# Optimization experiments

Hardware: AMD Instinct MI355X
Metric: run time of the kernel (lower is better)

The kernel has to match this reference:

```python
import jax, jax.numpy as jnp
import numpy as np

KERNEL = 7
DS_LIM = 0.01
ALPHA_M = 1.0


def _smooth_field(field):
    # field [3,D,H,W] -> depthwise mean filter with kernel 7, SAME padding
    k = KERNEL
    w = jnp.ones((3, 1, k, k, k), dtype=field.dtype) / (k ** 3)
    out = jax.lax.conv_general_dilated(
        field[None], w, (1, 1, 1), 'SAME',
        dimension_numbers=('NCDHW', 'OIDHW', 'NCDHW'),
        feature_group_count=3)
    return out[0]


def _trilinear(vol, coords):
    # vol [B,D,H,W]; coords [B,3,D,H,W] in voxel units
    B, D, H, W = vol.shape
    cz = jnp.clip(coords[:, 0], 0.0, D - 1.0)
    cy = jnp.clip(coords[:, 1], 0.0, H - 1.0)
    cx = jnp.clip(coords[:, 2], 0.0, W - 1.0)
    z0 = jnp.floor(cz).astype(jnp.int32); z1 = jnp.minimum(z0 + 1, D - 1)
    y0 = jnp.floor(cy).astype(jnp.int32); y1 = jnp.minimum(y0 + 1, H - 1)
    x0 = jnp.floor(cx).astype(jnp.int32); x1 = jnp.minimum(x0 + 1, W - 1)
    fz = cz - z0; fy = cy - y0; fx = cx - x0
    b = jnp.arange(B)[:, None, None, None]
    g = lambda zi, yi, xi: vol[b, zi, yi, xi]
    c00 = g(z0, y0, x0) * (1 - fx) + g(z0, y0, x1) * fx
    c01 = g(z0, y1, x0) * (1 - fx) + g(z0, y1, x1) * fx
    c10 = g(z1, y0, x0) * (1 - fx) + g(z1, y0, x1) * fx
    c11 = g(z1, y1, x0) * (1 - fx) + g(z1, y1, x1) * fx
    c0 = c00 * (1 - fy) + c01 * fy
    c1 = c10 * (1 - fy) + c11 * fy
    return c0 * (1 - fz) + c1 * fz


def setup_inputs() -> dict:
    key = jax.random.key(0)
    ks = jax.random.split(key, 8)
    B, C, L = 8, 128, 5
    D = H = W = 96
    return {
        'encode_ds': jax.random.normal(ks[0], (B, C, L, L, L), jnp.float32),
        'orig': jax.random.normal(ks[1], (B, 1, D, H, W), jnp.float32),
        'mask': jax.random.uniform(ks[2], (B, 1, D, H, W), jnp.float32),
        'c1_w': jax.random.normal(ks[3], (1, C, 1, 1, 1), jnp.float32) * 0.05,
        'c1_b': jnp.zeros((1,), jnp.float32),
        'f1_w': jax.random.normal(ks[4], (1, L ** 3), jnp.float32) * 0.1,
        'f1_b': jnp.zeros((1,), jnp.float32),
        'offset_field': jax.random.normal(ks[5], (3, D, H, W), jnp.float32),
    }


def reference(encode_ds, orig, mask, c1_w, c1_b, f1_w, f1_b, offset_field):
    B = encode_ds.shape[0]
    # 1x1x1 Conv3d (128 -> 1) is a per-voxel channel contraction
    a = jnp.einsum('bcdhw,c->bdhw', encode_ds, c1_w[0, :, 0, 0, 0]) + c1_b[0]
    a = a.reshape(B, -1)                                   # [B, 125]
    alpha = jax.nn.sigmoid(a @ f1_w[0] + f1_b[0]) * ALPHA_M  # [B]

    # deform: smoothed, ds_lim-clamped offset field scaled by per-sample alpha
    field = jnp.clip(_smooth_field(offset_field), -DS_LIM, DS_LIM)  # [3,D,H,W]
    _, _, D, H, W = orig.shape
    base = jnp.stack(jnp.meshgrid(jnp.arange(D, dtype=orig.dtype),
                                  jnp.arange(H, dtype=orig.dtype),
                                  jnp.arange(W, dtype=orig.dtype),
                                  indexing='ij'))          # [3,D,H,W]
    scale = jnp.array([D, H, W], orig.dtype).reshape(1, 3, 1, 1, 1)
    disp = alpha[:, None, None, None, None] * field[None] * scale  # [B,3,D,H,W]
    coords = base[None] + disp

    def_ = _trilinear(orig[:, 0], coords)[:, None]
    mask_d = _trilinear(mask[:, 0], coords)[:, None]
    return def_, mask_d
```

## Files before the change

kernel.cpp:

```cpp
#include <hip/hip_runtime.h>
#include <hip/hip_fp16.h>
#include <math.h>

#define DD 96
#define VOX (96*96*96)
#define NB 8
#define NC 128
#define L3 125

#define BTS 16
#define BNT 6
#define BNTILE (BNT*BNT*BNT)
#define BHS 22
#define YBS 23

#define TZ 12
#define TY 8
#define TX 32
#define NTZ 8
#define NTY 12
#define NTX 3
#define STILE (NTZ*NTY*NTX)
#define HZS 14
#define HYS 10
#define HXS 34
#define HXP 35
#define HN (HZS*HYS*HXS)
#define HLDS (HZS*HYS*HXP)

typedef float vfloat2 __attribute__((ext_vector_type(2)));

static __device__ __forceinline__ vfloat2 h2f(__half2 h) {
    float2 t = __half22float2(h);
    vfloat2 r; r.x = t.x; r.y = t.y;
    return r;
}

__global__ __launch_bounds__(256) void blur_alpha(
        const float* __restrict__ in, float* __restrict__ out,
        const float* __restrict__ enc,
        const float* __restrict__ c1_w, const float* __restrict__ c1_b,
        const float* __restrict__ f1_w, const float* __restrict__ f1_b,
        float* __restrict__ alpha) {
    __shared__ float h[BHS * BHS * BHS];
    __shared__ float zb[BTS * BHS * BHS];
    __shared__ float red[4];
    float* yb = h;
    int tid = threadIdx.x;

    if (blockIdx.x >= 3 * BNTILE) {
        int b = blockIdx.x - 3 * BNTILE;
        const float4* e4 = (const float4*)(enc + (size_t)b * NC * L3);
        float s = 0.f;
        for (int j = tid; j < (NC * L3) / 4; j += 256) {
            float4 v = e4[j];
            int f = j * 4;
            s += v.x * c1_w[(f + 0) / L3] * f1_w[(f + 0) % L3];
            s += v.y * c1_w[(f + 1) / L3] * f1_w[(f + 1) % L3];
            s += v.z * c1_w[(f + 2) / L3] * f1_w[(f + 2) % L3];
            s += v.w * c1_w[(f + 3) / L3] * f1_w[(f + 3) % L3];
        }
        for (int off = 32; off > 0; off >>= 1) s += __shfl_down(s, off, 64);
        int lane = tid & 63, wid = tid >> 6;
        if (lane == 0) red[wid] = s;
        __syncthreads();
        if (tid == 0) {
            float tot = red[0] + red[1] + red[2] + red[3];
            float fwsum = 0.f;
            for (int v = 0; v < L3; ++v) fwsum += f1_w[v];
            float x = tot + c1_b[0] * fwsum + f1_b[0];
            alpha[b] = 1.f / (1.f + expf(-x));
        }
        return;
    }

    int blk = blockIdx.x;
    int c = blk / BNTILE;
    int t = blk % BNTILE;
    int tz = t / (BNT * BNT), ty = (t / BNT) % BNT, tx = t % BNT;
    int bz = tz * BTS, by = ty * BTS, bx = tx * BTS;
    const float* ib = in + (size_t)c * VOX;

    for (int i = tid; i < BHS * BHS * BHS; i += 256) {
        int hz = i / (BHS * BHS);
        int hy = (i / BHS) % BHS;
        int hx = i % BHS;
        int gz = bz + hz - 3, gy = by + hy - 3, gx = bx + hx - 3;
        float v = 0.f;
        if (gz >= 0 && gz < DD && gy >= 0 && gy < DD && gx >= 0 && gx < DD)
            v = ib[(gz * DD + gy) * DD + gx];
        h[i] = v;
    }
    __syncthreads();

    for (int cc = tid; cc < BHS * BHS; cc += 256) {
        float s = 0.f;
        #pragma unroll
        for (int z = 0; z < 7; ++z) s += h[z * (BHS * BHS) + cc];
        zb[cc] = s;
        for (int z = 1; z < BTS; ++z) {
            s += h[(z + 6) * (BHS * BHS) + cc] - h[(z - 1) * (BHS * BHS) + cc];
            zb[z * (BHS * BHS) + cc] = s;
        }
    }
    __syncthreads();

    for (int cc = tid; cc < BTS * BHS; cc += 256) {
        int z = cc / BHS, hx = cc % BHS;
        const float* zp = zb + z * (BHS * BHS) + hx;
        float s = 0.f;
        #pragma unroll
        for (int y = 0; y < 7; ++y) s += zp[y * BHS];
        yb[(z * BTS) * YBS + hx] = s;
        for (int y = 1; y < BTS; ++y) {
            s += zp[(y + 6) * BHS] - zp[(y - 1) * BHS];
            yb[(z * BTS + y) * YBS + hx] = s;
        }
    }
    __syncthreads();

    {
        int z = tid >> 4, y = tid & 15;
        const float* yp = yb + (z * BTS + y) * YBS;
        float* op = out + (size_t)c * VOX + ((bz + z) * DD + (by + y)) * DD + bx;
        float s = yp[0] + yp[1] + yp[2] + yp[3] + yp[4] + yp[5] + yp[6];
        #pragma unroll
        for (int xq = 0; xq < 4; ++xq) {
            float4 o4;
            #pragma unroll
            for (int j = 0; j < 4; ++j) {
                int x = xq * 4 + j;
                float v = s * (1.0f / 343.0f);
                v = fminf(fmaxf(v, -0.01f), 0.01f) * 96.0f;
                if (j == 0) o4.x = v; else if (j == 1) o4.y = v;
                else if (j == 2) o4.z = v; else o4.w = v;
                if (x < BTS - 1) s += yp[x + 7] - yp[x];
            }
            ((float4*)op)[xq] = o4;
        }
    }
}

__global__ __launch_bounds__(256, 8) void sample_tile(
        const float* __restrict__ orig,
        const float* __restrict__ mask,
        const float* __restrict__ field,
        const float* __restrict__ alpha,
        float* __restrict__ out) {
    __shared__ __half2 tile[HLDS];

    int blk = blockIdx.x;
    int b = blk / STILE;
    int r = blk % STILE;
    int o = r & 7;
    int l = r >> 3;
    int zh = o >> 2;
    int yq = o & 3;
    int lz4 = l / 9, ly3 = (l / 3) % 3, lx3 = l % 3;
    int tz = zh * 4 + lz4;
    int ty = yq * 3 + ly3;
    int tx = lx3;
    int bz = tz * TZ, by = ty * TY, bx = tx * TX;

    const float* ob = orig + (size_t)b * VOX;
    const float* mb = mask + (size_t)b * VOX;
    int tid = threadIdx.x;

    for (int i = tid; i < HN; i += 256) {
        int hz = i / (HYS * HXS);
        int rr = i - hz * (HYS * HXS);
        int hy = rr / HXS;
        int hx = rr - hy * HXS;
        int gz = min(max(bz + hz - 1, 0), DD - 1);
        int gy = min(max(by + hy - 1, 0), DD - 1);
        int gx = min(max(bx + hx - 1, 0), DD - 1);
        int g = (gz * DD + gy) * DD + gx;
        tile[(hz * HYS + hy) * HXP + hx] = __floats2half2_rn(ob[g], mb[g]);
    }
    float a = alpha[b];
    __syncthreads();

    const float2* fz2 = (const float2*)field;
    const float2* fy2 = (const float2*)(field + VOX);
    const float2* fx2 = (const float2*)(field + 2 * VOX);
    vfloat2* oD = (vfloat2*)(out);
    vfloat2* oM = (vfloat2*)(out + (size_t)NB * VOX);

    int lz  = tid >> 7;
    int ly  = (tid >> 4) & 7;
    int lxp = tid & 15;
    int gy  = by + ly;
    int gx0 = bx + 2 * lxp;
    float gyf = (float)gy;
    float gx0f = (float)gx0, gx1f = (float)(gx0 + 1);
    float c1z = (float)(1 - bz), c1y = (float)(1 - by), c1x = (float)(1 - bx);

    auto samp = [&](float gzf, float dzv, float dyv, float dxv,
                    float gxf) -> vfloat2 {
        float cz = fminf(fmaxf(fmaf(a, dzv, gzf), 0.f), (float)(DD - 1)) + c1z;
        float cy = fminf(fmaxf(fmaf(a, dyv, gyf), 0.f), (float)(DD - 1)) + c1y;
        float cx = fminf(fmaxf(fmaf(a, dxv, gxf), 0.f), (float)(DD - 1)) + c1x;
        float flz = floorf(cz), fly = floorf(cy), flx = floorf(cx);
        float fzf = cz - flz, fyf = cy - fly, fxf = cx - flx;
        int iz = (int)flz, iy = (int)fly, ix = (int)flx;

        const __half2* tp = tile + (iz * HYS + iy) * HXP + ix;
        vfloat2 v000 = h2f(tp[0]);
        vfloat2 v001 = h2f(tp[1]);
        vfloat2 v010 = h2f(tp[HXP]);
        vfloat2 v011 = h2f(tp[HXP + 1]);
        vfloat2 v100 = h2f(tp[HYS * HXP]);
        vfloat2 v101 = h2f(tp[HYS * HXP + 1]);
        vfloat2 v110 = h2f(tp[(HYS + 1) * HXP]);
        vfloat2 v111 = h2f(tp[(HYS + 1) * HXP + 1]);

        vfloat2 FX = {fxf, fxf}, FY = {fyf, fyf}, FZ = {fzf, fzf};
        vfloat2 c00 = v000 + FX * (v001 - v000);
        vfloat2 c01 = v010 + FX * (v011 - v010);
        vfloat2 c10 = v100 + FX * (v101 - v100);
        vfloat2 c11 = v110 + FX * (v111 - v110);
        vfloat2 c0 = c00 + FY * (c01 - c00);
        vfloat2 c1 = c10 + FY * (c11 - c10);
        return c0 + FZ * (c1 - c0);
    };

    int vp = (((bz + lz) * DD + gy) * DD + gx0) >> 1;
    float2 dz = fz2[vp], dy = fy2[vp], dx = fx2[vp];
    size_t ob0 = (size_t)b * (VOX / 2);

    #pragma unroll
    for (int it = 0; it < TZ / 2; ++it) {
        float2 dzn = {0.f, 0.f}, dyn = {0.f, 0.f}, dxn = {0.f, 0.f};
        if (it < TZ / 2 - 1) {
            int vq = vp + DD * DD;
            dzn = fz2[vq]; dyn = fy2[vq]; dxn = fx2[vq];
        }
        float gzf = (float)(bz + 2 * it + lz);

        vfloat2 r0 = samp(gzf, dz.x, dy.x, dx.x, gx0f);
        vfloat2 r1 = samp(gzf, dz.y, dy.y, dx.y, gx1f);

        vfloat2 vD = {r0.x, r1.x};
        vfloat2 vM = {r0.y, r1.y};
        __builtin_nontemporal_store(vD, &oD[ob0 + vp]);
        __builtin_nontemporal_store(vM, &oM[ob0 + vp]);

        vp += DD * DD;
        dz = dzn; dy = dyn; dx = dxn;
    }
}

extern "C" void kernel_launch(void* const* d_in, const int* in_sizes, int n_in,
                              void* d_out, int out_size, void* d_ws, size_t ws_size,
                              hipStream_t stream) {
    const float* enc   = (const float*)d_in[0];
    const float* orig  = (const float*)d_in[1];
    const float* mask  = (const float*)d_in[2];
    const float* c1_w  = (const float*)d_in[3];
    const float* c1_b  = (const float*)d_in[4];
    const float* f1_w  = (const float*)d_in[5];
    const float* f1_b  = (const float*)d_in[6];
    const float* offs  = (const float*)d_in[7];
    float* out = (float*)d_out;

    float* ws = (float*)d_ws;
    float* alpha = ws;
    float* fieldB = ws + 16;

    blur_alpha<<<3 * BNTILE + NB, 256, 0, stream>>>(
        offs, fieldB, enc, c1_w, c1_b, f1_w, f1_b, alpha);
    sample_tile<<<NB * STILE, 256, 0, stream>>>(orig, mask, fieldB, alpha, out);
}
```

Baseline: 183.4 us.

## Restructure box blur as x-from-global then y/z in LDS; widen sampler to float4

The blur kernel now does the x-direction 7-tap sum straight from global memory into a smaller LDS buffer. It then does the y running sum in place, and the z running sum during the output write, which removes one LDS pass and one barrier and cuts the LDS footprint. The cost is more redundant global reads (7 per x-output), and the output stores become scalar and strided per z instead of float4. Separately, the sampling kernel now has each thread process 4 x-voxels with float4 field loads and float4 nontemporal stores, for fewer threads per z-slab and wider memory operations.

```diff
diff --git a/kernel.cpp b/kernel.cpp
--- a/kernel.cpp
+++ b/kernel.cpp
@@ -11,8 +11,9 @@
 #define BTS 16
 #define BNT 6
 #define BNTILE (BNT*BNT*BNT)
-#define BHS 22
-#define YBS 23
+#define BHZ 22
+#define BHY 22
+#define XSN (BHY * 23 * BTS)
 
 #define TZ 12
 #define TY 8
@@ -29,6 +30,7 @@
 #define HLDS (HZS*HYS*HXP)
 
 typedef float vfloat2 __attribute__((ext_vector_type(2)));
+typedef float vfloat4 __attribute__((ext_vector_type(4)));
 
 static __device__ __forceinline__ vfloat2 h2f(__half2 h) {
     float2 t = __half22float2(h);
@@ -42,10 +44,8 @@
         const float* __restrict__ c1_w, const float* __restrict__ c1_b,
         const float* __restrict__ f1_w, const float* __restrict__ f1_b,
         float* __restrict__ alpha) {
-    __shared__ float h[BHS * BHS * BHS];
-    __shared__ float zb[BTS * BHS * BHS];
+    __shared__ float xs[XSN];
     __shared__ float red[4];
-    float* yb = h;
     int tid = threadIdx.x;
 
     if (blockIdx.x >= 3 * BNTILE) {
@@ -81,62 +81,59 @@
     int bz = tz * BTS, by = ty * BTS, bx = tx * BTS;
     const float* ib = in + (size_t)c * VOX;
 
-    for (int i = tid; i < BHS * BHS * BHS; i += 256) {
-        int hz = i / (BHS * BHS);
-        int hy = (i / BHS) % BHS;
-        int hx = i % BHS;
-        int gz = bz + hz - 3, gy = by + hy - 3, gx = bx + hx - 3;
-        float v = 0.f;
-        if (gz >= 0 && gz < DD && gy >= 0 && gy < DD && gx >= 0 && gx < DD)
-            v = ib[(gz * DD + gy) * DD + gx];
-        h[i] = v;
+    bool xedge = (bx == 0) || (bx == DD - BTS);
+    for (int i = tid; i < BHY * BHZ * BTS; i += 256) {
+        int hy = i / (BHZ * BTS);
+        int r2 = i - hy * (BHZ * BTS);
+        int hz = r2 >> 4;
+        int xo = r2 & 15;
+        int gz = bz + hz - 3, gy = by + hy - 3;
+        float s = 0.f;
+        if ((unsigned)gz < DD && (unsigned)gy < DD) {
+            const float* p = ib + (gz * DD + gy) * DD + (bx + xo - 3);
+            if (!xedge) {
+                #pragma unroll
+                for (int dx = 0; dx < 7; ++dx) s += p[dx];
+            } else {
+                int gx0 = bx + xo - 3;
+                #pragma unroll
+                for (int dx = 0; dx < 7; ++dx)
+                    if ((unsigned)(gx0 + dx) < DD) s += p[dx];
+            }
+        }
+        xs[(hy * 23 + hz) * 16 + xo] = s;
     }
     __syncthreads();
 
-    for (int cc = tid; cc < BHS * BHS; cc += 256) {
-        float s = 0.f;
-        #pragma unroll
-        for (int z = 0; z < 7; ++z) s += h[z * (BHS * BHS) + cc];
-        zb[cc] = s;
-        for (int z = 1; z < BTS; ++z) {
-            s += h[(z + 6) * (BHS * BHS) + cc] - h[(z - 1) * (BHS * BHS) + cc];
-            zb[z * (BHS * BHS) + cc] = s;
+    for (int cc = tid; cc < BHZ * BTS; cc += 256) {
+        int hz = cc >> 4, xo = cc & 15;
+        int base = hz * 16 + xo;
+        float s = 0.f;
+        #pragma unroll
+        for (int hy = 0; hy < 7; ++hy) s += xs[hy * 368 + base];
+        #pragma unroll
+        for (int yo = 0; yo < 16; ++yo) {
+            float old = xs[yo * 368 + base];
+            float nxt = (yo < 15) ? xs[(yo + 7) * 368 + base] : 0.f;
+            xs[yo * 368 + base] = s;
+            s += nxt - old;
         }
     }
     __syncthreads();
 
-    for (int cc = tid; cc < BTS * BHS; cc += 256) {
-        int z = cc / BHS, hx = cc % BHS;
-        const float* zp = zb + z * (BHS * BHS) + hx;
-        float s = 0.f;
-        #pragma unroll
-        for (int y = 0; y < 7; ++y) s += zp[y * BHS];
-        yb[(z * BTS) * YBS + hx] = s;
-        for (int y = 1; y < BTS; ++y) {
-            s += zp[(y + 6) * BHS] - zp[(y - 1) * BHS];
-            yb[(z * BTS + y) * YBS + hx] = s;
-        }
-    }
-    __syncthreads();
-
     {
-        int z = tid >> 4, y = tid & 15;
-        const float* yp = yb + (z * BTS + y) * YBS;
-        float* op = out + (size_t)c * VOX + ((bz + z) * DD + (by + y)) * DD + bx;
-        float s = yp[0] + yp[1] + yp[2] + yp[3] + yp[4] + yp[5] + yp[6];
-        #pragma unroll
-        for (int xq = 0; xq < 4; ++xq) {
-            float4 o4;
-            #pragma unroll
-            for (int j = 0; j < 4; ++j) {
-                int x = xq * 4 + j;
-                float v = s * (1.0f / 343.0f);
-                v = fminf(fmaxf(v, -0.01f), 0.01f) * 96.0f;
-                if (j == 0) o4.x = v; else if (j == 1) o4.y = v;
-                else if (j == 2) o4.z = v; else o4.w = v;
-                if (x < BTS - 1) s += yp[x + 7] - yp[x];
-            }
-            ((float4*)op)[xq] = o4;
+        int yo = tid >> 4, xo = tid & 15;
+        int base = yo * 368 + xo;
+        float s = 0.f;
+        #pragma unroll
+        for (int hz = 0; hz < 7; ++hz) s += xs[base + hz * 16];
+        float* ob = out + (size_t)c * VOX + (by + yo) * DD + bx + xo;
+        #pragma unroll
+        for (int zo = 0; zo < 16; ++zo) {
+            float v = s * (1.0f / 343.0f);
+            v = fminf(fmaxf(v, -0.01f), 0.01f) * 96.0f;
+            ob[(size_t)(bz + zo) * DD * DD] = v;
+            s += xs[base + (zo + 7) * 16] - xs[base + zo * 16];
         }
     }
 }
@@ -180,19 +177,19 @@
     float a = alpha[b];
     __syncthreads();
 
-    const float2* fz2 = (const float2*)field;
-    const float2* fy2 = (const float2*)(field + VOX);
-    const float2* fx2 = (const float2*)(field + 2 * VOX);
-    vfloat2* oD = (vfloat2*)(out);
-    vfloat2* oM = (vfloat2*)(out + (size_t)NB * VOX);
-
-    int lz  = tid >> 7;
-    int ly  = (tid >> 4) & 7;
-    int lxp = tid & 15;
+    const vfloat4* fz4 = (const vfloat4*)field;
+    const vfloat4* fy4 = (const vfloat4*)(field + VOX);
+    const vfloat4* fx4 = (const vfloat4*)(field + 2 * VOX);
+    vfloat4* oD = (vfloat4*)(out);
+    vfloat4* oM = (vfloat4*)(out + (size_t)NB * VOX);
+
+    int lz  = tid >> 6;
+    int ly  = (tid >> 3) & 7;
+    int lxq = tid & 7;
     int gy  = by + ly;
-    int gx0 = bx + 2 * lxp;
+    int gx0 = bx + 4 * lxq;
     float gyf = (float)gy;
-    float gx0f = (float)gx0, gx1f = (float)(gx0 + 1);
+    float gx0f = (float)gx0;
     float c1z = (float)(1 - bz), c1y = (float)(1 - by), c1x = (float)(1 - bx);
 
     auto samp = [&](float gzf, float dzv, float dyv, float dxv,
@@ -224,28 +221,30 @@
         return c0 + FZ * (c1 - c0);
     };
 
-    int vp = (((bz + lz) * DD + gy) * DD + gx0) >> 1;
-    float2 dz = fz2[vp], dy = fy2[vp], dx = fx2[vp];
-    size_t ob0 = (size_t)b * (VOX / 2);
+    int vp4 = (((bz + lz) * DD + gy) * DD + gx0) >> 2;
+    vfloat4 dz = fz4[vp4], dy = fy4[vp4], dx = fx4[vp4];
+    size_t ob0 = (size_t)b * (VOX / 4);
 
     #pragma unroll
-    for (int it = 0; it < TZ / 2; ++it) {
-        float2 dzn = {0.f, 0.f}, dyn = {0.f, 0.f}, dxn = {0.f, 0.f};
-        if (it < TZ / 2 - 1) {
-            int vq = vp + DD * DD;
-            dzn = fz2[vq]; dyn = fy2[vq]; dxn = fx2[vq];
-        }
-        float gzf = (float)(bz + 2 * it + lz);
+    for (int it = 0; it < TZ / 4; ++it) {
+        vfloat4 dzn = {0,0,0,0}, dyn = {0,0,0,0}, dxn = {0,0,0,0};
+        if (it < TZ / 4 - 1) {
+            int vq = vp4 + DD * DD;
+            dzn = fz4[vq]; dyn = fy4[vq]; dxn = fx4[vq];
+        }
+        float gzf = (float)(bz + 4 * it + lz);
 
         vfloat2 r0 = samp(gzf, dz.x, dy.x, dx.x, gx0f);
-        vfloat2 r1 = samp(gzf, dz.y, dy.y, dx.y, gx1f);
-
-        vfloat2 vD = {r0.x, r1.x};
-        vfloat2 vM = {r0.y, r1.y};
-        __builtin_nontemporal_store(vD, &oD[ob0 + vp]);
-        __builtin_nontemporal_store(vM, &oM[ob0 + vp]);
-
-        vp += DD * DD;
+        vfloat2 r1 = samp(gzf, dz.y, dy.y, dx.y, gx0f + 1.f);
+        vfloat2 r2 = samp(gzf, dz.z, dy.z, dx.z, gx0f + 2.f);
+        vfloat2 r3 = samp(gzf, dz.w, dy.w, dx.w, gx0f + 3.f);
+
+        vfloat4 vD = {r0.x, r1.x, r2.x, r3.x};
+        vfloat4 vM = {r0.y, r1.y, r2.y, r3.y};
+        __builtin_nontemporal_store(vD, &oD[ob0 + vp4]);
+        __builtin_nontemporal_store(vM, &oM[ob0 + vp4]);
+
+        vp4 += DD * DD;
         dz = dzn; dy = dyn; dx = dxn;
     }
 }
```

Result: no change. 182.4 us (-0.5%).
